# Optimization experiments

Hardware: AMD Instinct MI355X
Metric: run time of the kernel (lower is better)

Reference implementation:

```python
import jax, jax.numpy as jnp
import numpy as np

D = 1024          # d_model
EXPAND = 2
DI = EXPAND * D   # d_inner = 2048
K = 4             # d_conv
B, L = 4, 2048
EPS = 1e-6


def setup_inputs() -> dict:
    key = jax.random.key(0)
    ks = jax.random.split(key, 16)
    n = lambda i, shape, scale=0.02: (jax.random.normal(ks[i], shape, jnp.float32) * scale)
    return {
        "x": jax.random.normal(ks[0], (B, L, D), jnp.float32),
        "norm_w": jnp.ones((D,), jnp.float32),
        "up_w": n(1, (D, DI)), "up_b": jnp.zeros((DI,), jnp.float32),
        "gate_w": n(2, (D, DI)), "gate_b": jnp.zeros((DI,), jnp.float32),
        "down_w": n(3, (DI, D)), "down_b": jnp.zeros((D,), jnp.float32),
        "conv_w": n(4, (DI, K), 0.2), "conv_b": jnp.zeros((DI,), jnp.float32),
        "wq": n(5, (D, D)), "wk": n(6, (D, D)), "wv": n(7, (D, D)), "wo": n(8, (D, D)),
        "decay": jnp.float32(0.99),
    }


def _rmsnorm(x, w):
    return x * jax.lax.rsqrt(jnp.mean(x * x, axis=-1, keepdims=True) + EPS) * w


def _forward(x, norm_w, up_w, up_b, gate_w, gate_b, down_w, down_b,
             conv_w, conv_b, wq, wk, wv, wo, decay):
    normed = _rmsnorm(x, norm_w)                              # [B,L,D]
    h = normed @ up_w + up_b                                  # [B,L,DI]
    # causal depthwise conv1d: left-pad K-1, groups = DI
    di = conv_w.shape[0]
    kern = conv_w.T[:, None, :]                               # [K,1,DI] (WIO)
    h = jax.lax.conv_general_dilated(
        h, kern, window_strides=(1,), padding=[(conv_w.shape[1] - 1, 0)],
        dimension_numbers=("NWC", "WIO", "NWC"), feature_group_count=di)
    h = jax.nn.silu(h + conv_b)                               # [B,L,DI]
    # gated MLP combine + down-projection
    out = (h * jax.nn.silu(normed @ gate_w + gate_b)) @ down_w + down_b  # [B,L,D]
    # Hebbian associative memory: M_t = decay*M_{t-1} + k_t^T v_t; y_t = q_t M_t
    q = out @ wq; k = out @ wk; v = out @ wv                  # [B,L,D]
    M0 = jnp.zeros((out.shape[0], out.shape[-1], out.shape[-1]), out.dtype)

    def step(M, qkv):
        qt, kt, vt = qkv                                      # each [B,D]
        M = decay * M + jnp.einsum("bd,be->bde", kt, vt)
        return M, jnp.einsum("bd,bde->be", qt, M)

    _, ys = jax.lax.scan(step, M0, (q.swapaxes(0, 1), k.swapaxes(0, 1), v.swapaxes(0, 1)))
    mem_out = ys.swapaxes(0, 1) @ wo                          # [B,L,D]
    return x + mem_out


def reference(x, norm_w, up_w, up_b, gate_w, gate_b, down_w, down_b,
              conv_w, conv_b, wq, wk, wv, wo, decay):
    return _forward(x, norm_w, up_w, up_b, gate_w, gate_b, down_w, down_b,
                    conv_w, conv_b, wq, wk, wv, wo, decay)
```

## Files before the change

### kernel.cpp

```cpp
#include <hip/hip_runtime.h>


typedef __bf16 bf16x8 __attribute__((ext_vector_type(8)));
typedef unsigned short u16x8 __attribute__((ext_vector_type(8)));
typedef float f32x4 __attribute__((ext_vector_type(4)));

constexpr int Bb = 4, Ll = 2048, Dd = 1024, DIc = 2048;
constexpr long LD  = (long)Ll * Dd;
constexpr long BLD = (long)Bb * LD;

static __device__ __forceinline__ unsigned short f2bf(float f) {
  unsigned u = __builtin_bit_cast(unsigned, f);
  u += 0x7fffu + ((u >> 16) & 1u);
  return (unsigned short)(u >> 16);
}
static __device__ __forceinline__ float bf2f(unsigned short u) {
  return __builtin_bit_cast(float, (unsigned)u << 16);
}
static __device__ __forceinline__ float silu(float g) {
  return g / (1.f + __expf(-g));
}

enum { EP_UG = 0, EP_DOWN, EP_QKV, EP_DECAY, EP_Y, EP_WO };

#define STAGE_A(DBUF, MG, KH, TILE) {                                          \
    const int kt_ = ((TILE) < NTm1 ? (TILE) : NTm1);                           \
    __builtin_amdgcn_global_load_lds(                                          \
      (const __attribute__((address_space(1))) void*)                          \
        (Ag + (size_t)(aRow + (MG)*64) * lda + kt_*64 + (KH)*32 + aCol),       \
      (__attribute__((address_space(3))) void*)                                \
        (lds + (DBUF)*ADB + (KH)*AKH + (aRb + (MG)*4)*512), 16, 0, 0); }

#define STAGE_B(DBUF, NH, KH, TILE) {                                          \
    const int kt_ = ((TILE) < NTm1 ? (TILE) : NTm1);                           \
    __builtin_amdgcn_global_load_lds(                                          \
      (const __attribute__((address_space(1))) void*)                          \
        (Bg + (size_t)(bRow + (NH)*128) * ldb + kt_*64 + (KH)*32 + aCol),      \
      (__attribute__((address_space(3))) void*)                                \
        (lds + BOFF + (DBUF)*16384 + (KH)*8192 + ((NH)*8 + w)*512), 16, 0, 0); }

#define LOAD_A(DBUF, KS, MG) {                                                 \
  _Pragma("unroll") for (int j_ = 0; j_ < 4; ++j_)                             \
    af[j_] = *(const bf16x8*)&lds[(DBUF)*ADB + (KS)*AKH +                      \
        (aRdBase + (MG)*4 + j_)*512 + fr*32 + cph]; }

#define LOAD_B(DBUF, KS) {                                                     \
  _Pragma("unroll") for (int n_ = 0; n_ < 4; ++n_)                             \
    bfr[KS][n_] = *(const bf16x8*)&lds[BOFF + (DBUF)*16384 + (KS)*8192 +       \
        (bRb + n_)*512 + fr*32 + cph]; }

#define MFMA_PH(KS, MG) {                                                      \
  __builtin_amdgcn_s_setprio(1);                                               \
  _Pragma("unroll") for (int j_ = 0; j_ < 4; ++j_)                             \
  _Pragma("unroll") for (int n_ = 0; n_ < 4; ++n_)                             \
    acc[(MG)*4 + j_][n_] = __builtin_amdgcn_mfma_f32_16x16x32_bf16(            \
        af[j_], bfr[KS][n_], acc[(MG)*4 + j_][n_], 0, 0, 0);                   \
  __builtin_amdgcn_s_setprio(0); }

#define BAR() __builtin_amdgcn_s_barrier()
#define WAIT_LGKM0() { asm volatile("s_waitcnt lgkmcnt(0)" ::: "memory");      \
                       __builtin_amdgcn_sched_barrier(0); }
#define WAIT_LGKM8() asm volatile("s_waitcnt lgkmcnt(8)" ::: "memory")
#define WAIT_VM(N) asm volatile("s_waitcnt vmcnt(" #N ")" ::: "memory")

template <int EPI, int BM>
__global__ __launch_bounds__(512, 2) void gemm8_k(
    const ushort* __restrict__ A, const ushort* __restrict__ Bm,
    void* __restrict__ O0, const float* __restrict__ bias,
    const float* __restrict__ bias2, const float* __restrict__ xres,
    const float* __restrict__ decayp,
    int K, int lda, int ldb, int ldc,
    long sA, long sB, long sC,
    void* __restrict__ O1, void* __restrict__ O2) {
  constexpr int MF = BM / 32;
  constexpr int ADB = BM * 64;
  constexpr int AKH = BM * 32;
  constexpr int BOFF = BM * 128;
  __shared__ ushort lds[BM == 256 ? 65536 : 49152];

  const int z = blockIdx.z;
  const int gx = gridDim.x;
  const int nwg = gx * gridDim.y;
  const int id = blockIdx.y * gx + blockIdx.x;
  const int chunk = nwg >> 3;
  const int swz = (id & 7) * chunk + (id >> 3);
  const int m0 = (swz / gx) * BM;
  const int n0 = (swz % gx) * 256;

  const int t = threadIdx.x;
  const int lane = t & 63;
  const int w = t >> 6;

  if constexpr (EPI == EP_DECAY) {
    if (n0 > m0) {
      ushort* S = (ushort*)O0 + (size_t)z * sC;
      u16x8 zz = {};
#pragma unroll
      for (int i = 0; i < BM / 16; ++i) {
        const int cid = i * 512 + t;
        *(u16x8*)&S[(size_t)(m0 + (cid >> 5)) * ldc + n0 + (cid & 31) * 8] = zz;
      }
      return;
    }
  }

  const ushort* Ag = A + (size_t)z * sA + (size_t)m0 * lda;
  const ushort* Bg = Bm + (size_t)z * sB + (size_t)n0 * ldb;

  int Kend = K;
  if constexpr (EPI == EP_Y) Kend = (K < m0 + BM) ? K : m0 + BM;
  const int NT = Kend >> 6;
  const int NTm1 = NT - 1;
  const int NI = NT >> 1;

  const int lp = lane ^ (((lane >> 5) & 1) << 1);
  const int aCol = (lp & 3) * 8;
  const int bRow = (w >> 2) * 64 + (w & 3) * 16 + (lp >> 2);
  int aRow, aRb, aRdBase;
  if constexpr (BM == 256) {
    aRow = (w >> 2) * 128 + (w & 3) * 16 + (lp >> 2);
    aRb = (w >> 2) * 8 + (w & 3);
    aRdBase = (w >> 2) * 8;
  } else {
    aRow = w * 16 + (lp >> 2);
    aRb = w;
    aRdBase = (w >> 2) * 4;
  }
  const int fr = lane & 15;
  const int kg = (lane >> 4) * 8;
  const int cph = kg ^ (((fr >> 3) & 1) << 4);
  const int bRb = ((w & 3) >> 1) * 8 + ((w & 3) & 1) * 4;

  f32x4 acc[MF][4] = {};
  bf16x8 af[4], bfr[2][4];

  if constexpr (BM == 256) {
    STAGE_A(0, 0, 0, 0); STAGE_A(0, 0, 1, 0); STAGE_A(0, 1, 0, 0); STAGE_A(0, 1, 1, 0);
    STAGE_B(0, 0, 0, 0); STAGE_B(0, 0, 1, 0); STAGE_B(0, 1, 0, 0); STAGE_B(0, 1, 1, 0);
    STAGE_B(1, 0, 0, 1); STAGE_B(1, 0, 1, 1); STAGE_B(1, 1, 0, 1); STAGE_B(1, 1, 1, 1);
    STAGE_A(1, 0, 0, 1); STAGE_A(1, 0, 1, 1);
    WAIT_VM(6);
    BAR();
    for (int i = 0; i < NI; ++i) {
      const int tt = 2 * i;
      LOAD_B(0, 0); LOAD_B(0, 1); LOAD_A(0, 0, 0);
      STAGE_A(1, 1, 0, tt + 1); STAGE_A(1, 1, 1, tt + 1);
      WAIT_LGKM8();
      BAR(); WAIT_LGKM0();
      MFMA_PH(0, 0);
      BAR();
      LOAD_A(0, 0, 1);
      STAGE_B(0, 0, 0, tt + 2); STAGE_B(0, 1, 0, tt + 2);
      BAR(); WAIT_LGKM0();
      MFMA_PH(0, 1);
      BAR();
      LOAD_A(0, 1, 0);
      STAGE_B(0, 0, 1, tt + 2); STAGE_B(0, 1, 1, tt + 2);
      BAR(); WAIT_LGKM0();
      MFMA_PH(1, 0);
      BAR();
      LOAD_A(0, 1, 1);
      STAGE_A(0, 0, 0, tt + 2); STAGE_A(0, 0, 1, tt + 2);
      WAIT_VM(6);
      BAR(); WAIT_LGKM0();
      MFMA_PH(1, 1);
      BAR();
      LOAD_B(1, 0); LOAD_B(1, 1); LOAD_A(1, 0, 0);
      STAGE_A(0, 1, 0, tt + 2); STAGE_A(0, 1, 1, tt + 2);
      WAIT_LGKM8();
      BAR(); WAIT_LGKM0();
      MFMA_PH(0, 0);
      BAR();
      LOAD_A(1, 0, 1);
      STAGE_B(1, 0, 0, tt + 3); STAGE_B(1, 1, 0, tt + 3);
      BAR(); WAIT_LGKM0();
      MFMA_PH(0, 1);
      BAR();
      LOAD_A(1, 1, 0);
      STAGE_B(1, 0, 1, tt + 3); STAGE_B(1, 1, 1, tt + 3);
      BAR(); WAIT_LGKM0();
      MFMA_PH(1, 0);
      BAR();
      LOAD_A(1, 1, 1);
      STAGE_A(1, 0, 0, tt + 3); STAGE_A(1, 0, 1, tt + 3);
      WAIT_VM(6);
      BAR(); WAIT_LGKM0();
      MFMA_PH(1, 1);
      BAR();
    }
  } else {
    STAGE_A(0, 0, 0, 0); STAGE_A(0, 0, 1, 0);
    STAGE_B(0, 0, 0, 0); STAGE_B(0, 1, 0, 0); STAGE_B(0, 0, 1, 0); STAGE_B(0, 1, 1, 0);
    STAGE_B(1, 0, 0, 1); STAGE_B(1, 1, 0, 1); STAGE_B(1, 0, 1, 1); STAGE_B(1, 1, 1, 1);
    WAIT_VM(4);
    BAR();
    for (int i = 0; i < NI; ++i) {
      const int tt = 2 * i;
      LOAD_B(0, 0); LOAD_B(0, 1); LOAD_A(0, 0, 0);
      STAGE_A(1, 0, 0, tt + 1); STAGE_A(1, 0, 1, tt + 1);
      WAIT_LGKM8();
      BAR(); WAIT_LGKM0();
      MFMA_PH(0, 0);
      BAR();
      LOAD_A(0, 1, 0);
      STAGE_B(0, 0, 0, tt + 2); STAGE_B(0, 1, 0, tt + 2);
      STAGE_B(0, 0, 1, tt + 2); STAGE_B(0, 1, 1, tt + 2);
      WAIT_VM(4);
      BAR(); WAIT_LGKM0();
      MFMA_PH(1, 0);
      BAR();
      LOAD_B(1, 0); LOAD_B(1, 1); LOAD_A(1, 0, 0);
      STAGE_A(0, 0, 0, tt + 2); STAGE_A(0, 0, 1, tt + 2);
      WAIT_LGKM8();
      BAR(); WAIT_LGKM0();
      MFMA_PH(0, 0);
      BAR();
      LOAD_A(1, 1, 0);
      STAGE_B(1, 0, 0, tt + 3); STAGE_B(1, 1, 0, tt + 3);
      STAGE_B(1, 0, 1, tt + 3); STAGE_B(1, 1, 1, tt + 3);
      WAIT_VM(4);
      BAR(); WAIT_LGKM0();
      MFMA_PH(1, 0);
      BAR();
    }
  }

  const int rb4 = (lane >> 4) * 4;
  const int wm = (w >> 2) * (BM / 2), wn = (w & 3) * 64;
  float logd = 0.f;
  if constexpr (EPI == EP_DECAY) logd = __logf(decayp[0]);

#pragma unroll
  for (int mf = 0; mf < MF; ++mf) {
#pragma unroll
    for (int nf = 0; nf < 4; ++nf) {
      const int gm0 = m0 + wm + mf * 16 + rb4;
      const int gn = n0 + wn + nf * 16 + fr;
      if constexpr (EPI == EP_QKV) {
        if (gn < 2048) {
          ushort* dst = (gn < 1024) ? (ushort*)O0 : (ushort*)O1;
          const int col = gn & 1023;
#pragma unroll
          for (int r = 0; r < 4; ++r)
            dst[(size_t)(gm0 + r) * 1024 + col] = f2bf(acc[mf][nf][r]);
        } else {
          const int d = gn - 2048, b = gm0 >> 11, ttp = gm0 & 2047;
          ushort4 w4;
          w4.x = f2bf(acc[mf][nf][0]); w4.y = f2bf(acc[mf][nf][1]);
          w4.z = f2bf(acc[mf][nf][2]); w4.w = f2bf(acc[mf][nf][3]);
          *(ushort4*)&((ushort*)O2)[(size_t)b * LD + (size_t)d * Ll + ttp] = w4;
        }
      } else {
#pragma unroll
        for (int r = 0; r < 4; ++r) {
          const int gm = gm0 + r;
          const size_t idx = (size_t)z * sC + (size_t)gm * ldc + gn;
          const float v = acc[mf][nf][r];
          if constexpr (EPI == EP_UG) {
            const float b = (gn < 2048) ? bias[gn] : bias2[gn - 2048];
            ((ushort*)O0)[idx] = f2bf(v + b);
          } else if constexpr (EPI == EP_DOWN) {
            ((ushort*)O0)[idx] = f2bf(v + bias[gn]);
          } else if constexpr (EPI == EP_DECAY) {
            ((ushort*)O0)[idx] =
                (gn <= gm) ? f2bf(v * __expf((float)(gm - gn) * logd)) : (ushort)0;
          } else if constexpr (EPI == EP_Y) {
            ((ushort*)O0)[idx] = f2bf(v);
          } else {
            ((float*)O0)[idx] = v + xres[idx];
          }
        }
      }
    }
  }
}

__global__ __launch_bounds__(256) void prep_k(
    const float* __restrict__ up_w, const float* __restrict__ gate_w,
    const float* __restrict__ down_w, const float* __restrict__ wq,
    const float* __restrict__ wk, const float* __restrict__ wv,
    const float* __restrict__ wo, const float* __restrict__ conv_w,
    const float* __restrict__ x, const float* __restrict__ norm_w,
    ushort* __restrict__ ugw, ushort* __restrict__ down_wT,
    ushort* __restrict__ qkv_wT, ushort* __restrict__ wo_T,
    ushort* __restrict__ cwT, ushort* __restrict__ nrm) {
  const int bid = blockIdx.x;
  const int t = threadIdx.x;
  if (bid < 10240) {
    const float* src; ushort* dst; int R, C, idx;
    if (bid < 2048)      { src = up_w;   dst = ugw;                R = 1024; C = 2048; idx = bid; }
    else if (bid < 4096) { src = gate_w; dst = ugw + 2048 * 1024;  R = 1024; C = 2048; idx = bid - 2048; }
    else if (bid < 6144) { src = down_w; dst = down_wT;            R = 2048; C = 1024; idx = bid - 4096; }
    else if (bid < 7168) { src = wq;     dst = qkv_wT;             R = 1024; C = 1024; idx = bid - 6144; }
    else if (bid < 8192) { src = wk;     dst = qkv_wT + 1024*1024; R = 1024; C = 1024; idx = bid - 7168; }
    else if (bid < 9216) { src = wv;     dst = qkv_wT + 2*1024*1024; R = 1024; C = 1024; idx = bid - 8192; }
    else                 { src = wo;     dst = wo_T;               R = 1024; C = 1024; idx = bid - 9216; }
    __shared__ float tile[32][33];
    const int tx = t & 31, ty = t >> 5;
    const int tilesx = C >> 5;
    const int c0 = (idx % tilesx) * 32, r0 = (idx / tilesx) * 32;
#pragma unroll
    for (int i = 0; i < 4; ++i)
      tile[ty + i * 8][tx] = src[(size_t)(r0 + ty + i * 8) * C + c0 + tx];
    __syncthreads();
#pragma unroll
    for (int i = 0; i < 4; ++i)
      dst[(size_t)(c0 + ty + i * 8) * R + r0 + tx] = f2bf(tile[tx][ty + i * 8]);
  } else if (bid < 10248) {
    const int c = (bid - 10240) * 256 + t;
    const float4 v = *(const float4*)(conv_w + c * 4);
    cwT[0 * DIc + c] = f2bf(v.x);
    cwT[1 * DIc + c] = f2bf(v.y);
    cwT[2 * DIc + c] = f2bf(v.z);
    cwT[3 * DIc + c] = f2bf(v.w);
  } else {
    const int row = bid - 10248;
    const float* xr = x + (size_t)row * Dd;
    const float4 v = *(const float4*)(xr + t * 4);
    float ss = v.x * v.x + v.y * v.y + v.z * v.z + v.w * v.w;
#pragma unroll
    for (int m = 32; m; m >>= 1) ss += __shfl_xor(ss, m);
    __shared__ float red[4];
    if ((t & 63) == 0) red[t >> 6] = ss;
    __syncthreads();
    const float total = red[0] + red[1] + red[2] + red[3];
    const float rs = rsqrtf(total * (1.f / (float)Dd) + 1e-6f);
    const float4 wt = *(const float4*)(norm_w + t * 4);
    ushort4 r;
    r.x = f2bf(v.x * rs * wt.x); r.y = f2bf(v.y * rs * wt.y);
    r.z = f2bf(v.z * rs * wt.z); r.w = f2bf(v.w * rs * wt.w);
    *(ushort4*)(nrm + (size_t)row * Dd + t * 4) = r;
  }
}

__global__ __launch_bounds__(256) void conv_gate_k(
    const ushort* __restrict__ ug, const ushort* __restrict__ cwT,
    const float* __restrict__ cb, ushort* __restrict__ o) {
  const int t = threadIdx.x;
  const int cg = t & 31;
  const int ts = t >> 5;
  const int cblk = blockIdx.x & 7;
  const int rblk = blockIdx.x >> 3;
  const int c = cblk * 256 + cg * 8;
  const int row0 = rblk * 64 + ts * 8;

  u16x8 w[4];
#pragma unroll
  for (int k = 0; k < 4; ++k) w[k] = *(const u16x8*)&cwT[k * DIc + c];
  float wb[8];
  *(float4*)&wb[0] = *(const float4*)(cb + c);
  *(float4*)&wb[4] = *(const float4*)(cb + c + 4);

  u16x8 h3, h2, h1;
  if ((row0 & (Ll - 1)) == 0) {
    h3 = (u16x8){}; h2 = (u16x8){}; h1 = (u16x8){};
  } else {
    h3 = *(const u16x8*)&ug[(size_t)(row0 - 3) * 4096 + c];
    h2 = *(const u16x8*)&ug[(size_t)(row0 - 2) * 4096 + c];
    h1 = *(const u16x8*)&ug[(size_t)(row0 - 1) * 4096 + c];
  }

#pragma unroll
  for (int i = 0; i < 8; ++i) {
    const size_t rbase = (size_t)(row0 + i) * 4096;
    const u16x8 h0 = *(const u16x8*)&ug[rbase + c];
    const u16x8 g  = *(const u16x8*)&ug[rbase + 2048 + c];
    u16x8 ov;
#pragma unroll
    for (int j = 0; j < 8; ++j) {
      float acc = wb[j];
      acc += bf2f(w[0][j]) * bf2f(h3[j]);
      acc += bf2f(w[1][j]) * bf2f(h2[j]);
      acc += bf2f(w[2][j]) * bf2f(h1[j]);
      acc += bf2f(w[3][j]) * bf2f(h0[j]);
      ov[j] = f2bf(silu(acc) * silu(bf2f(g[j])));
    }
    *(u16x8*)&o[(size_t)(row0 + i) * DIc + c] = ov;
    h3 = h2; h2 = h1; h1 = h0;
  }
}

extern "C" void kernel_launch(void* const* d_in, const int* in_sizes, int n_in,
                              void* d_out, int out_size, void* d_ws,
                              size_t ws_size, hipStream_t stream) {
  const float* x      = (const float*)d_in[0];
  const float* norm_w = (const float*)d_in[1];
  const float* up_w   = (const float*)d_in[2];
  const float* up_b   = (const float*)d_in[3];
  const float* gate_w = (const float*)d_in[4];
  const float* gate_b = (const float*)d_in[5];
  const float* down_w = (const float*)d_in[6];
  const float* down_b = (const float*)d_in[7];
  const float* conv_w = (const float*)d_in[8];
  const float* conv_b = (const float*)d_in[9];
  const float* wq     = (const float*)d_in[10];
  const float* wk     = (const float*)d_in[11];
  const float* wv     = (const float*)d_in[12];
  const float* wo     = (const float*)d_in[13];
  const float* decay  = (const float*)d_in[14];
  float* out = (float*)d_out;
  char* w8 = (char*)d_ws;

  const size_t MiB = 1u << 20;
  ushort* nrm      = (ushort*)(w8 + 0 * MiB);
  ushort* ug       = (ushort*)(w8 + 16 * MiB);
  ushort* S        = (ushort*)(w8 + 16 * MiB);
  ushort* combined = (ushort*)(w8 + 80 * MiB);
  ushort* buf1     = (ushort*)(w8 + 112 * MiB);
  ushort* buf2     = (ushort*)(w8 + 144 * MiB);
  ushort* ugw      = (ushort*)(w8 + 176 * MiB);
  ushort* down_wT  = (ushort*)(w8 + 184 * MiB);
  ushort* qkv_wT   = (ushort*)(w8 + 188 * MiB);
  ushort* wo_T     = (ushort*)(w8 + 194 * MiB);
  ushort* cwT      = (ushort*)(w8 + 196 * MiB);

  ushort* q  = buf1;
  ushort* kb = buf1 + BLD;
  ushort* vT = buf2;
  ushort* y  = buf2 + BLD;

  prep_k<<<18440, 256, 0, stream>>>(up_w, gate_w, down_w, wq, wk, wv, wo,
                                    conv_w, x, norm_w,
                                    ugw, down_wT, qkv_wT, wo_T, cwT, nrm);

  gemm8_k<EP_UG, 256><<<dim3(16, 32), 512, 0, stream>>>(
      nrm, ugw, ug, up_b, gate_b, nullptr, nullptr,
      1024, 1024, 1024, 4096, 0, 0, 0, nullptr, nullptr);

  conv_gate_k<<<1024, 256, 0, stream>>>(ug, cwT, conv_b, combined);

  gemm8_k<EP_DOWN, 128><<<dim3(4, 64), 512, 0, stream>>>(
      combined, down_wT, nrm, down_b, nullptr, nullptr, nullptr,
      2048, 2048, 2048, 1024, 0, 0, 0, nullptr, nullptr);

  gemm8_k<EP_QKV, 128><<<dim3(12, 64), 512, 0, stream>>>(
      nrm, qkv_wT, q, nullptr, nullptr, nullptr, nullptr,
      1024, 1024, 1024, 1024, 0, 0, 0, kb, vT);

  gemm8_k<EP_DECAY, 256><<<dim3(8, 8, Bb), 512, 0, stream>>>(
      q, kb, S, nullptr, nullptr, nullptr, decay,
      1024, 1024, 1024, 2048, LD, LD, (long)Ll * Ll, nullptr, nullptr);

  gemm8_k<EP_Y, 128><<<dim3(4, 16, Bb), 512, 0, stream>>>(
      S, vT, y, nullptr, nullptr, nullptr, nullptr,
      2048, 2048, 2048, 1024, (long)Ll * Ll, LD, LD, nullptr, nullptr);

  gemm8_k<EP_WO, 128><<<dim3(4, 64), 512, 0, stream>>>(
      y, wo_T, out, nullptr, nullptr, x, nullptr,
      1024, 1024, 1024, 1024, 0, 0, 0, nullptr, nullptr);
}
```

Measured before the change: 323.7 us.

## Fold q/k and v/wo projections into precomputed weight products

Reassociates the memory computation: rather than projecting q, k and v separately, it precomputes Ws = Wq·Wk^T and Wv2 = Wv·Wo as small extra GEMMs in a second z-slice of the up/gate launch. Then G = out·Ws and out·Wv2 come from a single GEMM, the decay GEMM uses G against out directly, and the final wo GEMM is fused into the S·V GEMM together with the residual add. This drops one 1024-wide projection and the whole wo GEMM launch, and also skips zeroing the upper-triangle S tiles. The cost is extra bf16 rounding from the precomputed weight products, plus the assumption that the skipped upper-triangle S tiles are never read because the Y GEMM's K range is bounded.

```diff
diff --git a/kernel.cpp b/kernel.cpp
--- a/kernel.cpp
+++ b/kernel.cpp
@@ -21,7 +21,7 @@
   return g / (1.f + __expf(-g));
 }
 
-enum { EP_UG = 0, EP_DOWN, EP_QKV, EP_DECAY, EP_Y, EP_WO };
+enum { EP_UG = 0, EP_DOWN, EP_GV, EP_DECAY, EP_YO };
 
 #define STAGE_A(DBUF, MG, KH, TILE) {                                          \
     const int kt_ = ((TILE) < NTm1 ? (TILE) : NTm1);                           \
@@ -71,7 +71,11 @@
     const float* __restrict__ decayp,
     int K, int lda, int ldb, int ldc,
     long sA, long sB, long sC,
-    void* __restrict__ O1, void* __restrict__ O2) {
+    void* __restrict__ O1,
+    const ushort* __restrict__ sA1, const ushort* __restrict__ sB1,
+    ushort* __restrict__ sC1,
+    const ushort* __restrict__ sA2, const ushort* __restrict__ sB2,
+    ushort* __restrict__ sC2) {
   constexpr int MF = BM / 32;
   constexpr int ADB = BM * 64;
   constexpr int AKH = BM * 32;
@@ -84,31 +88,38 @@
   const int id = blockIdx.y * gx + blockIdx.x;
   const int chunk = nwg >> 3;
   const int swz = (id & 7) * chunk + (id >> 3);
-  const int m0 = (swz / gx) * BM;
-  const int n0 = (swz % gx) * 256;
+  int m0 = (swz / gx) * BM;
+  int n0 = (swz % gx) * 256;
 
   const int t = threadIdx.x;
   const int lane = t & 63;
   const int w = t >> 6;
 
+  bool small = false;
+  ushort* Cs = nullptr;
+  const ushort* Ag;
+  const ushort* Bg;
+  if constexpr (EPI == EP_UG) {
+    if (z == 1) {
+      if (id >= 32) return;
+      const int lid = id & 15;
+      m0 = (lid >> 2) * 256;
+      n0 = (lid & 3) * 256;
+      if (id < 16) { Ag = sA1 + (size_t)m0 * 1024; Bg = sB1 + (size_t)n0 * 1024; Cs = sC1; }
+      else         { Ag = sA2 + (size_t)m0 * 1024; Bg = sB2 + (size_t)n0 * 1024; Cs = sC2; }
+      small = true;
+    }
+  }
   if constexpr (EPI == EP_DECAY) {
-    if (n0 > m0) {
-      ushort* S = (ushort*)O0 + (size_t)z * sC;
-      u16x8 zz = {};
-#pragma unroll
-      for (int i = 0; i < BM / 16; ++i) {
-        const int cid = i * 512 + t;
-        *(u16x8*)&S[(size_t)(m0 + (cid >> 5)) * ldc + n0 + (cid & 31) * 8] = zz;
-      }
-      return;
-    }
-  }
-
-  const ushort* Ag = A + (size_t)z * sA + (size_t)m0 * lda;
-  const ushort* Bg = Bm + (size_t)z * sB + (size_t)n0 * ldb;
+    if (n0 > m0) return;
+  }
+  if (!small) {
+    Ag = A + (size_t)z * sA + (size_t)m0 * lda;
+    Bg = Bm + (size_t)z * sB + (size_t)n0 * ldb;
+  }
 
   int Kend = K;
-  if constexpr (EPI == EP_Y) Kend = (K < m0 + BM) ? K : m0 + BM;
+  if constexpr (EPI == EP_YO) Kend = (K < m0 + BM) ? K : m0 + BM;
   const int NT = Kend >> 6;
   const int NTm1 = NT - 1;
   const int NI = NT >> 1;
@@ -236,19 +247,17 @@
     for (int nf = 0; nf < 4; ++nf) {
       const int gm0 = m0 + wm + mf * 16 + rb4;
       const int gn = n0 + wn + nf * 16 + fr;
-      if constexpr (EPI == EP_QKV) {
-        if (gn < 2048) {
-          ushort* dst = (gn < 1024) ? (ushort*)O0 : (ushort*)O1;
-          const int col = gn & 1023;
+      if constexpr (EPI == EP_GV) {
+        if (gn < 1024) {
 #pragma unroll
           for (int r = 0; r < 4; ++r)
-            dst[(size_t)(gm0 + r) * 1024 + col] = f2bf(acc[mf][nf][r]);
+            ((ushort*)O0)[(size_t)(gm0 + r) * 1024 + gn] = f2bf(acc[mf][nf][r]);
         } else {
-          const int d = gn - 2048, b = gm0 >> 11, ttp = gm0 & 2047;
+          const int d = gn - 1024, b = gm0 >> 11, ttp = gm0 & 2047;
           ushort4 w4;
           w4.x = f2bf(acc[mf][nf][0]); w4.y = f2bf(acc[mf][nf][1]);
           w4.z = f2bf(acc[mf][nf][2]); w4.w = f2bf(acc[mf][nf][3]);
-          *(ushort4*)&((ushort*)O2)[(size_t)b * LD + (size_t)d * Ll + ttp] = w4;
+          *(ushort4*)&((ushort*)O1)[(size_t)b * LD + (size_t)d * Ll + ttp] = w4;
         }
       } else {
 #pragma unroll
@@ -257,15 +266,17 @@
           const size_t idx = (size_t)z * sC + (size_t)gm * ldc + gn;
           const float v = acc[mf][nf][r];
           if constexpr (EPI == EP_UG) {
-            const float b = (gn < 2048) ? bias[gn] : bias2[gn - 2048];
-            ((ushort*)O0)[idx] = f2bf(v + b);
+            if (small) {
+              Cs[(size_t)gm * 1024 + gn] = f2bf(v);
+            } else {
+              const float b = (gn < 2048) ? bias[gn] : bias2[gn - 2048];
+              ((ushort*)O0)[idx] = f2bf(v + b);
+            }
           } else if constexpr (EPI == EP_DOWN) {
             ((ushort*)O0)[idx] = f2bf(v + bias[gn]);
           } else if constexpr (EPI == EP_DECAY) {
             ((ushort*)O0)[idx] =
                 (gn <= gm) ? f2bf(v * __expf((float)(gm - gn) * logd)) : (ushort)0;
-          } else if constexpr (EPI == EP_Y) {
-            ((ushort*)O0)[idx] = f2bf(v);
           } else {
             ((float*)O0)[idx] = v + xres[idx];
           }
@@ -282,19 +293,17 @@
     const float* __restrict__ wo, const float* __restrict__ conv_w,
     const float* __restrict__ x, const float* __restrict__ norm_w,
     ushort* __restrict__ ugw, ushort* __restrict__ down_wT,
-    ushort* __restrict__ qkv_wT, ushort* __restrict__ wo_T,
+    ushort* __restrict__ wq_bf, ushort* __restrict__ wk_bf,
+    ushort* __restrict__ wv_bf, ushort* __restrict__ wo_T,
     ushort* __restrict__ cwT, ushort* __restrict__ nrm) {
   const int bid = blockIdx.x;
   const int t = threadIdx.x;
-  if (bid < 10240) {
+  if (bid < 7168) {
     const float* src; ushort* dst; int R, C, idx;
-    if (bid < 2048)      { src = up_w;   dst = ugw;                R = 1024; C = 2048; idx = bid; }
-    else if (bid < 4096) { src = gate_w; dst = ugw + 2048 * 1024;  R = 1024; C = 2048; idx = bid - 2048; }
-    else if (bid < 6144) { src = down_w; dst = down_wT;            R = 2048; C = 1024; idx = bid - 4096; }
-    else if (bid < 7168) { src = wq;     dst = qkv_wT;             R = 1024; C = 1024; idx = bid - 6144; }
-    else if (bid < 8192) { src = wk;     dst = qkv_wT + 1024*1024; R = 1024; C = 1024; idx = bid - 7168; }
-    else if (bid < 9216) { src = wv;     dst = qkv_wT + 2*1024*1024; R = 1024; C = 1024; idx = bid - 8192; }
-    else                 { src = wo;     dst = wo_T;               R = 1024; C = 1024; idx = bid - 9216; }
+    if (bid < 2048)      { src = up_w;   dst = ugw;               R = 1024; C = 2048; idx = bid; }
+    else if (bid < 4096) { src = gate_w; dst = ugw + 2048 * 1024; R = 1024; C = 2048; idx = bid - 2048; }
+    else if (bid < 6144) { src = down_w; dst = down_wT;           R = 2048; C = 1024; idx = bid - 4096; }
+    else                 { src = wo;     dst = wo_T;              R = 1024; C = 1024; idx = bid - 6144; }
     __shared__ float tile[32][33];
     const int tx = t & 31, ty = t >> 5;
     const int tilesx = C >> 5;
@@ -306,6 +315,16 @@
 #pragma unroll
     for (int i = 0; i < 4; ++i)
       dst[(size_t)(c0 + ty + i * 8) * R + r0 + tx] = f2bf(tile[tx][ty + i * 8]);
+  } else if (bid < 10240) {
+    const int seg = (bid - 7168) >> 10;
+    const int idx = (bid - 7168) & 1023;
+    const float* src = (seg == 0) ? wq : (seg == 1) ? wk : wv;
+    ushort* dst = (seg == 0) ? wq_bf : (seg == 1) ? wk_bf : wv_bf;
+    const size_t e = (size_t)idx * 1024 + t * 4;
+    const float4 v = *(const float4*)(src + e);
+    ushort4 r;
+    r.x = f2bf(v.x); r.y = f2bf(v.y); r.z = f2bf(v.z); r.w = f2bf(v.w);
+    *(ushort4*)(dst + e) = r;
   } else if (bid < 10248) {
     const int c = (bid - 10240) * 256 + t;
     const float4 v = *(const float4*)(conv_w + c * 4);
@@ -406,46 +425,47 @@
   ushort* ug       = (ushort*)(w8 + 16 * MiB);
   ushort* S        = (ushort*)(w8 + 16 * MiB);
   ushort* combined = (ushort*)(w8 + 80 * MiB);
-  ushort* buf1     = (ushort*)(w8 + 112 * MiB);
-  ushort* buf2     = (ushort*)(w8 + 144 * MiB);
+  ushort* G        = (ushort*)(w8 + 112 * MiB);
+  ushort* vT       = (ushort*)(w8 + 144 * MiB);
   ushort* ugw      = (ushort*)(w8 + 176 * MiB);
   ushort* down_wT  = (ushort*)(w8 + 184 * MiB);
-  ushort* qkv_wT   = (ushort*)(w8 + 188 * MiB);
+  ushort* wq_bf    = (ushort*)(w8 + 188 * MiB);
+  ushort* wk_bf    = (ushort*)(w8 + 190 * MiB);
+  ushort* wv_bf    = (ushort*)(w8 + 192 * MiB);
   ushort* wo_T     = (ushort*)(w8 + 194 * MiB);
-  ushort* cwT      = (ushort*)(w8 + 196 * MiB);
-
-  ushort* q  = buf1;
-  ushort* kb = buf1 + BLD;
-  ushort* vT = buf2;
-  ushort* y  = buf2 + BLD;
+  ushort* WsT      = (ushort*)(w8 + 196 * MiB);
+  ushort* Wv2T     = (ushort*)(w8 + 198 * MiB);
+  ushort* cwT      = (ushort*)(w8 + 200 * MiB);
 
   prep_k<<<18440, 256, 0, stream>>>(up_w, gate_w, down_w, wq, wk, wv, wo,
                                     conv_w, x, norm_w,
-                                    ugw, down_wT, qkv_wT, wo_T, cwT, nrm);
-
-  gemm8_k<EP_UG, 256><<<dim3(16, 32), 512, 0, stream>>>(
+                                    ugw, down_wT, wq_bf, wk_bf, wv_bf, wo_T,
+                                    cwT, nrm);
+
+  gemm8_k<EP_UG, 256><<<dim3(16, 32, 2), 512, 0, stream>>>(
       nrm, ugw, ug, up_b, gate_b, nullptr, nullptr,
-      1024, 1024, 1024, 4096, 0, 0, 0, nullptr, nullptr);
+      1024, 1024, 1024, 4096, 0, 0, 0, nullptr,
+      wk_bf, wq_bf, WsT, wo_T, wv_bf, Wv2T);
 
   conv_gate_k<<<1024, 256, 0, stream>>>(ug, cwT, conv_b, combined);
 
   gemm8_k<EP_DOWN, 128><<<dim3(4, 64), 512, 0, stream>>>(
       combined, down_wT, nrm, down_b, nullptr, nullptr, nullptr,
-      2048, 2048, 2048, 1024, 0, 0, 0, nullptr, nullptr);
-
-  gemm8_k<EP_QKV, 128><<<dim3(12, 64), 512, 0, stream>>>(
-      nrm, qkv_wT, q, nullptr, nullptr, nullptr, nullptr,
-      1024, 1024, 1024, 1024, 0, 0, 0, kb, vT);
+      2048, 2048, 2048, 1024, 0, 0, 0, nullptr,
+      nullptr, nullptr, nullptr, nullptr, nullptr, nullptr);
+
+  gemm8_k<EP_GV, 128><<<dim3(8, 64), 512, 0, stream>>>(
+      nrm, WsT, G, nullptr, nullptr, nullptr, nullptr,
+      1024, 1024, 1024, 1024, 0, 0, 0, vT,
+      nullptr, nullptr, nullptr, nullptr, nullptr, nullptr);
 
   gemm8_k<EP_DECAY, 256><<<dim3(8, 8, Bb), 512, 0, stream>>>(
-      q, kb, S, nullptr, nullptr, nullptr, decay,
-      1024, 1024, 1024, 2048, LD, LD, (long)Ll * Ll, nullptr, nullptr);
-
-  gemm8_k<EP_Y, 128><<<dim3(4, 16, Bb), 512, 0, stream>>>(
-      S, vT, y, nullptr, nullptr, nullptr, nullptr,
-      2048, 2048, 2048, 1024, (long)Ll * Ll, LD, LD, nullptr, nullptr);
-
-  gemm8_k<EP_WO, 128><<<dim3(4, 64), 512, 0, stream>>>(
-      y, wo_T, out, nullptr, nullptr, x, nullptr,
-      1024, 1024, 1024, 1024, 0, 0, 0, nullptr, nullptr);
-}
+      G, nrm, S, nullptr, nullptr, nullptr, decay,
+      1024, 1024, 1024, 2048, LD, LD, (long)Ll * Ll, nullptr,
+      nullptr, nullptr, nullptr, nullptr, nullptr, nullptr);
+
+  gemm8_k<EP_YO, 128><<<dim3(4, 16, Bb), 512, 0, stream>>>(
+      S, vT, out, nullptr, nullptr, x, nullptr,
+      2048, 2048, 2048, 1024, (long)Ll * Ll, LD, LD, nullptr,
+      nullptr, nullptr, nullptr, nullptr, nullptr, nullptr);
+}
```

After: 322.3 us. About the same (-0.4%).
